# Kernel tuning notes

Hardware: AMD Instinct MI355X
Metric: run time of the kernel (lower is better)

Reference implementation:

```python
import math
import jax, jax.numpy as jnp
import numpy as np

D = 1024
NH = 16
DH = D // NH


def setup_inputs() -> dict:
    key = jax.random.key(0)
    k1, k2, k3 = jax.random.split(key, 3)
    x = jax.random.normal(k1, (2, 2048, D), dtype=jnp.float32)
    s = 1.0 / math.sqrt(D)
    W_qkv = jax.random.normal(k2, (D, 3 * D), dtype=jnp.float32) * s
    W_o = jax.random.normal(k3, (D, D), dtype=jnp.float32) * s
    return {"x": x, "W_qkv": W_qkv, "W_o": W_o}


def _rope(q, k, base=10000.0):
    # q, k: [B, H, T, dh]
    half = q.shape[-1] // 2
    freqs = jnp.arange(half, dtype=q.dtype) / half
    theta = 1.0 / base ** freqs                      # [half]
    t = jnp.arange(q.shape[-2], dtype=q.dtype)       # [T]
    ang = t[:, None] * theta[None, :]                # [T, half]
    cos = jnp.cos(ang)[None, None, :, :]
    sin = jnp.sin(ang)[None, None, :, :]

    def rot(x):
        x1, x2 = x[..., :half], x[..., half:]
        return jnp.concatenate([x1 * cos - x2 * sin, x1 * sin + x2 * cos], axis=-1)

    return rot(q), rot(k)


def reference(x, W_qkv, W_o):
    B, T, d = x.shape
    qkv = x @ W_qkv                                   # [B, T, 3D]
    q, k, v = jnp.split(qkv, 3, axis=-1)
    q = q.reshape(B, T, NH, DH).transpose(0, 2, 1, 3)  # [B, H, T, dh]
    k = k.reshape(B, T, NH, DH).transpose(0, 2, 1, 3)
    v = v.reshape(B, T, NH, DH).transpose(0, 2, 1, 3)
    q, k = _rope(q, k)
    att = jnp.einsum('bhtd,bhsd->bhts', q, k) / math.sqrt(DH)  # [B, H, T, T]
    mask = jnp.triu(jnp.full((T, T), -jnp.inf, dtype=att.dtype), 1)
    att = att + mask
    w = jax.nn.softmax(att, axis=-1)
    y = jnp.einsum('bhts,bhsd->bhtd', w, v)           # [B, H, T, dh]
    y = y.transpose(0, 2, 1, 3).reshape(B, T, d)
    return y @ W_o
```

## Files before the change

### kernel.cpp

```cpp
#include <hip/hip_runtime.h>

typedef __bf16 bf16x8 __attribute__((ext_vector_type(8)));
typedef float f32x4 __attribute__((ext_vector_type(4)));
typedef float f32x16 __attribute__((ext_vector_type(16)));

constexpr int SEQ = 2048;
constexpr int DMODEL = 1024;

#define GLL(gp, lp)                                                              \
  __builtin_amdgcn_global_load_lds((const __attribute__((address_space(1))) void*)(gp), \
                                   (__attribute__((address_space(3))) void*)(lp), 16, 0, 0)

__global__ __launch_bounds__(256) void prep_kernel(const float* __restrict__ x,
                                                   const float* __restrict__ Wqkv,
                                                   const float* __restrict__ Wo,
                                                   __bf16* __restrict__ xbf,
                                                   __bf16* __restrict__ WqkvT,
                                                   __bf16* __restrict__ WoT,
                                                   float2* __restrict__ sct) {
  __shared__ __bf16 tile[64][72];
  int blk = blockIdx.x, t = threadIdx.x;

  if (blk < 256) {
    int i = blk * 256 + t;
    int tt = i >> 5, j = i & 31;
    float theta = exp2f(-(float)j * 0.41524101186092953f);
    float s, c;
    __sincosf((float)tt * theta, &s, &c);
    sct[i] = make_float2(c, s);
    return;
  }
  if (blk >= 1280) {
    size_t i = (size_t)(blk - 1280) * 256 + t;
    const float* sp = x + i * 8;
    float4 f0 = *reinterpret_cast<const float4*>(sp);
    float4 f1 = *reinterpret_cast<const float4*>(sp + 4);
    alignas(16) __bf16 tmp[8];
    tmp[0] = (__bf16)f0.x; tmp[1] = (__bf16)f0.y; tmp[2] = (__bf16)f0.z; tmp[3] = (__bf16)f0.w;
    tmp[4] = (__bf16)f1.x; tmp[5] = (__bf16)f1.y; tmp[6] = (__bf16)f1.z; tmp[7] = (__bf16)f1.w;
    *reinterpret_cast<uint4*>(xbf + i * 8) = *reinterpret_cast<const uint4*>(tmp);
    return;
  }
  const float* src;
  __bf16* dst;
  int C, R, c0, r0;
  if (blk < 512) {
    int idx = blk - 256;
    src = Wo; dst = WoT; R = 1024; C = 1024;
    c0 = (idx & 15) * 64; r0 = (idx >> 4) * 64;
  } else {
    int idx = blk - 512;
    src = Wqkv; dst = WqkvT; R = 1024; C = 3072;
    c0 = (idx % 48) * 64; r0 = (idx / 48) * 64;
  }
#pragma unroll
  for (int p = 0; p < 2; ++p) {
    int flat = p * 256 + t;
    int i = flat >> 3;
    int j8 = (flat & 7) * 8;
    const float* sp = &src[(size_t)(r0 + i) * C + c0 + j8];
    float4 f0 = *reinterpret_cast<const float4*>(sp);
    float4 f1 = *reinterpret_cast<const float4*>(sp + 4);
    tile[i][j8 + 0] = (__bf16)f0.x; tile[i][j8 + 1] = (__bf16)f0.y;
    tile[i][j8 + 2] = (__bf16)f0.z; tile[i][j8 + 3] = (__bf16)f0.w;
    tile[i][j8 + 4] = (__bf16)f1.x; tile[i][j8 + 5] = (__bf16)f1.y;
    tile[i][j8 + 6] = (__bf16)f1.z; tile[i][j8 + 7] = (__bf16)f1.w;
  }
  __syncthreads();
#pragma unroll
  for (int p = 0; p < 2; ++p) {
    int flat = p * 256 + t;
    int i = flat >> 3;
    int j8 = (flat & 7) * 8;
    alignas(16) __bf16 tmp[8];
#pragma unroll
    for (int jj = 0; jj < 8; ++jj) tmp[jj] = tile[j8 + jj][i];
    *reinterpret_cast<uint4*>(&dst[(size_t)(c0 + i) * R + r0 + j8]) =
        *reinterpret_cast<const uint4*>(tmp);
  }
}

template <typename CT, int BN, int MODE>
__global__ __launch_bounds__(512, 6) void gemm_bt_lds(const __bf16* __restrict__ A,
                                                      const __bf16* __restrict__ BT,
                                                      CT* __restrict__ C,
                                                      int M, int N, int K, int lda, int ldc,
                                                      const float2* __restrict__ sct,
                                                      __bf16* __restrict__ vt) {
  constexpr int NF = BN / 32;
  __shared__ __align__(16) __bf16 AB_lds[128 + BN][64];
  __bf16 (*A_lds)[64] = &AB_lds[0];
  __bf16 (*B_lds)[64] = &AB_lds[128];

  int tid = threadIdx.x;
  int lane = tid & 63, w = tid >> 6;
  int g = lane >> 4, l15 = lane & 15;
  int wr = w & 3;
  int wc = w >> 2;
  int m0 = blockIdx.x * 128;
  int n0 = blockIdx.y * BN;
  int r8 = lane >> 3, scol = (lane & 7) * 8;

  const __bf16* ag = A + (size_t)(m0 + w * 16 + r8) * lda + scol;
  const __bf16* bg = BT + (size_t)(n0 + w * (BN / 8) + r8) * K + scol;

  f32x4 acc[2][NF] = {};

  for (int k0 = 0; k0 < K; k0 += 64) {
    __syncthreads();
    GLL(ag + k0, &A_lds[w * 16][0]);
    GLL(ag + (size_t)8 * lda + k0, &A_lds[w * 16 + 8][0]);
    if constexpr (BN == 128) {
      GLL(bg + k0, &B_lds[w * 16][0]);
      GLL(bg + (size_t)8 * K + k0, &B_lds[w * 16 + 8][0]);
    } else {
      GLL(bg + k0, &B_lds[w * 8][0]);
    }
    __syncthreads();
#pragma unroll
    for (int kk = 0; kk < 2; ++kk) {
      bf16x8 a[2], bb[NF];
#pragma unroll
      for (int m = 0; m < 2; ++m)
        a[m] = *reinterpret_cast<const bf16x8*>(&A_lds[wr * 32 + m * 16 + l15][kk * 32 + g * 8]);
#pragma unroll
      for (int n = 0; n < NF; ++n)
        bb[n] = *reinterpret_cast<const bf16x8*>(&B_lds[wc * (BN / 2) + n * 16 + l15][kk * 32 + g * 8]);
#pragma unroll
      for (int m = 0; m < 2; ++m)
#pragma unroll
        for (int n = 0; n < NF; ++n)
          acc[m][n] = __builtin_amdgcn_mfma_f32_16x16x32_bf16(a[m], bb[n], acc[m][n], 0, 0, 0);
    }
  }

  if constexpr (MODE == 3) {
    if (n0 >= 2048) {
      __bf16 (*T_lds)[72] = reinterpret_cast<__bf16(*)[72]>(&AB_lds[0][0]);
      int b = m0 >> 11;
      int s_base = m0 & (SEQ - 1);
#pragma unroll
      for (int half = 0; half < 2; ++half) {
        __syncthreads();
        if (wc == half) {
#pragma unroll
          for (int m = 0; m < 2; ++m)
#pragma unroll
            for (int n = 0; n < NF; ++n)
#pragma unroll
              for (int r = 0; r < 4; ++r)
                T_lds[wr * 32 + m * 16 + 4 * g + r][n * 16 + l15] = (__bf16)acc[m][n][r];
        }
        __syncthreads();
        int head = ((n0 - 2048) >> 6) + half;
        int bh = b * 16 + head;
        int d = tid >> 3;
        int s8 = (tid & 7) * 16;
        __bf16* dst = vt + (size_t)bh * 64 * SEQ + (size_t)d * SEQ + s_base + s8;
#pragma unroll
        for (int j = 0; j < 2; ++j) {
          alignas(16) __bf16 tmp[8];
#pragma unroll
          for (int e = 0; e < 8; ++e) tmp[e] = T_lds[s8 + j * 8 + e][d];
          *reinterpret_cast<uint4*>(dst + j * 8) = *reinterpret_cast<const uint4*>(tmp);
        }
      }
      return;
    }
    bool isq = (n0 < 1024);
    float sc = isq ? 0.18033688011112042f : 1.0f;
#pragma unroll
    for (int m = 0; m < 2; ++m)
#pragma unroll
      for (int r = 0; r < 4; ++r) {
        int row = m0 + wr * 32 + m * 16 + 4 * g + r;
        int t = row & (SEQ - 1);
#pragma unroll
        for (int n = 0; n < 2; ++n) {
          int j = n * 16 + l15;
          float2 cs = sct[(t << 5) + j];
          float x1 = acc[m][n][r], x2 = acc[m][n + 2][r];
          acc[m][n][r]     = (x1 * cs.x - x2 * cs.y) * sc;
          acc[m][n + 2][r] = (x1 * cs.y + x2 * cs.x) * sc;
        }
      }
  }

#pragma unroll
  for (int m = 0; m < 2; ++m)
#pragma unroll
    for (int n = 0; n < NF; ++n)
#pragma unroll
      for (int r = 0; r < 4; ++r) {
        int row = m0 + wr * 32 + m * 16 + 4 * g + r;
        int col = n0 + wc * (BN / 2) + n * 16 + l15;
        C[(size_t)row * ldc + col] = (CT)acc[m][n][r];
      }
}

__device__ inline uint32_t pkbf(float a, float b) {
  union { __bf16 h[2]; uint32_t u; } z;
  z.h[0] = (__bf16)a; z.h[1] = (__bf16)b;
  return z.u;
}

__device__ inline __bf16* slot_base(int gi, __bf16* qkv, __bf16* xbf, int q_local) {
  if (gi < 1024)
    return qkv + (size_t)(gi * 4 + (q_local >> 4)) * 3072 + 2048 + (q_local & 15) * 64;
  return xbf + (size_t)(gi - 1024) * 4096 + (size_t)q_local * 64;
}

__global__ __launch_bounds__(128, 3) void attn_kernel(__bf16* __restrict__ qkv,
                                                      const __bf16* __restrict__ vt,
                                                      __bf16* __restrict__ xbf,
                                                      float* __restrict__ pml) {
  __shared__ __align__(16) __bf16 K_lds[2][64][64];

  int tid = threadIdx.x;
  int w = tid >> 6, lane = tid & 63;
  int l31 = lane & 31, hi = lane >> 5;
  int bid = blockIdx.x;
  int it = bid >> 5, bh = bid & 31;
  int b = bh >> 4, h = bh & 15;

  int qc = 31 - (it >> 1);
  int half = it & 1;
  int NTf = qc + 1;
  int hs = (NTf + 1) >> 1;
  int kv0 = half ? hs : 0;
  int kv1 = half ? NTf : hs;
  int NT = kv1 - kv0;

  __bf16* qbase = qkv + (size_t)b * SEQ * 3072 + h * 64;
  const __bf16* kbase = qbase + 1024;
  const __bf16* vtb = vt + (size_t)bh * 64 * SEQ;

  int q_g = qc * 64 + w * 32 + l31;

  int r8 = lane >> 3;
  int cxe = 8 * ((lane & 7) ^ r8);

  auto STAGE = [&](int bufv, int t) {
#pragma unroll
    for (int i = 0; i < 4; ++i) {
      int R = w * 32 + i * 8;
      GLL(kbase + (size_t)(t * 64 + R + r8) * 3072 + cxe, &K_lds[bufv][R][0]);
    }
  };

  bf16x8 qf[4];
#pragma unroll
  for (int ds = 0; ds < 4; ++ds)
    qf[ds] = *reinterpret_cast<const bf16x8*>(qbase + (size_t)q_g * 3072 + ds * 16 + 8 * hi);

  f32x16 oacc[2] = {};
  float l_run = 0.f;
  const float MFIX = 8.0f;

  if (NT > 0) STAGE(0, kv0);
  __syncthreads();

  int buf = 0;
  for (int jb = 0; jb < NT; ++jb) {
    int kt_g = kv0 + jb;
    bool pre = (jb + 1 < NT);
    if (pre) STAGE(buf ^ 1, kt_g + 1);

    uint4 vr[8];
#pragma unroll
    for (int dt = 0; dt < 2; ++dt)
#pragma unroll
      for (int ks = 0; ks < 4; ++ks)
        vr[dt * 4 + ks] = *reinterpret_cast<const uint4*>(
            vtb + (size_t)(dt * 32 + l31) * SEQ + kt_g * 64 + ks * 16 + 8 * hi);

    f32x16 sacc[2] = {};
    __builtin_amdgcn_s_setprio(1);
#pragma unroll
    for (int kt = 0; kt < 2; ++kt) {
#pragma unroll
      for (int ds = 0; ds < 4; ++ds) {
        bf16x8 kf = *reinterpret_cast<const bf16x8*>(
            &K_lds[buf][kt * 32 + l31][(ds * 16 + 8 * hi) ^ ((l31 & 7) * 8)]);
        sacc[kt] = __builtin_amdgcn_mfma_f32_32x32x16_bf16(kf, qf[ds], sacc[kt], 0, 0, 0);
      }
    }
    __builtin_amdgcn_s_setprio(0);

    if (kt_g == qc) {
#pragma unroll
      for (int kt = 0; kt < 2; ++kt)
#pragma unroll
        for (int r = 0; r < 16; ++r) {
          int k_g = kt_g * 64 + kt * 32 + (r & 3) + 8 * (r >> 2) + 4 * hi;
          if (k_g > q_g) sacc[kt][r] = -1e30f;
        }
    }

    float s0 = 0.f, s1 = 0.f, s2 = 0.f, s3 = 0.f;
#pragma unroll
    for (int kt = 0; kt < 2; ++kt) {
#pragma unroll
      for (int r = 0; r < 16; r += 4) {
        float p0 = exp2f(sacc[kt][r + 0] - MFIX);
        float p1 = exp2f(sacc[kt][r + 1] - MFIX);
        float p2 = exp2f(sacc[kt][r + 2] - MFIX);
        float p3 = exp2f(sacc[kt][r + 3] - MFIX);
        sacc[kt][r + 0] = p0; sacc[kt][r + 1] = p1;
        sacc[kt][r + 2] = p2; sacc[kt][r + 3] = p3;
        s0 += p0; s1 += p1; s2 += p2; s3 += p3;
      }
    }
    float sum = (s0 + s1) + (s2 + s3);
    sum += __shfl_xor(sum, 32);
    l_run += sum;

    uint4 pa[4];
#pragma unroll
    for (int ks = 0; ks < 4; ++ks) {
      int v0 = 2 * ks, v1 = v0 + 1;
      int t0 = v0 >> 2, rb0 = 4 * (v0 & 3);
      int t1 = v1 >> 2, rb1 = 4 * (v1 & 3);
      uint32_t a01, a23, b01, b23;
      if (t0 == 0) { a01 = pkbf(sacc[0][rb0 + 0], sacc[0][rb0 + 1]);
                     a23 = pkbf(sacc[0][rb0 + 2], sacc[0][rb0 + 3]); }
      else         { a01 = pkbf(sacc[1][rb0 + 0], sacc[1][rb0 + 1]);
                     a23 = pkbf(sacc[1][rb0 + 2], sacc[1][rb0 + 3]); }
      if (t1 == 0) { b01 = pkbf(sacc[0][rb1 + 0], sacc[0][rb1 + 1]);
                     b23 = pkbf(sacc[0][rb1 + 2], sacc[0][rb1 + 3]); }
      else         { b01 = pkbf(sacc[1][rb1 + 0], sacc[1][rb1 + 1]);
                     b23 = pkbf(sacc[1][rb1 + 2], sacc[1][rb1 + 3]); }
      uint32_t t01 = hi ? a01 : b01;
      uint32_t t23 = hi ? a23 : b23;
      uint32_t r01 = __shfl_xor(t01, 32);
      uint32_t r23 = __shfl_xor(t23, 32);
      uint32_t k01 = hi ? b01 : a01;
      uint32_t k23 = hi ? b23 : a23;
      pa[ks].x = hi ? r01 : k01;
      pa[ks].y = hi ? r23 : k23;
      pa[ks].z = hi ? k01 : r01;
      pa[ks].w = hi ? k23 : r23;
    }

    __builtin_amdgcn_s_setprio(1);
#pragma unroll
    for (int dt = 0; dt < 2; ++dt) {
#pragma unroll
      for (int ks = 0; ks < 4; ++ks) {
        oacc[dt] = __builtin_amdgcn_mfma_f32_32x32x16_bf16(
            *reinterpret_cast<const bf16x8*>(&vr[dt * 4 + ks]),
            *reinterpret_cast<const bf16x8*>(&pa[ks]), oacc[dt], 0, 0, 0);
      }
    }
    __builtin_amdgcn_s_setprio(0);

    if (pre) {
      asm volatile("s_waitcnt vmcnt(0)" ::: "memory");
      __syncthreads();
    }
    buf ^= 1;
  }

  int gi = ((31 - qc) * 2 + half) * 32 + bh;
  int q_local = w * 32 + l31;
  __bf16* pobase = slot_base(gi, qkv, xbf, q_local);
#pragma unroll
  for (int dt = 0; dt < 2; ++dt)
#pragma unroll
    for (int u = 0; u < 4; ++u) {
      int d0 = dt * 32 + 8 * u + 4 * hi;
      alignas(8) __bf16 tmp[4];
#pragma unroll
      for (int m = 0; m < 4; ++m) tmp[m] = (__bf16)oacc[dt][4 * u + m];
      *reinterpret_cast<uint2*>(pobase + d0) = *reinterpret_cast<const uint2*>(tmp);
    }
  if (hi == 0) pml[gi * 128 + q_local] = l_run;
}

__global__ __launch_bounds__(128) void combine_kernel(__bf16* __restrict__ qkv,
                                                      __bf16* __restrict__ xbf,
                                                      const float* __restrict__ pml) {
  int bid = blockIdx.x;
  int qc = 31 - (bid >> 5), bh = bid & 31;
  int b = bh >> 4, h = bh & 15;
  int t = threadIdx.x;
  int q = t >> 1, dh = (t & 1) * 32;

  int g0 = ((31 - qc) * 2 + 0) * 32 + bh;
  int g1 = g0 + 32;
  float l0 = pml[g0 * 128 + q];
  float l1 = pml[g1 * 128 + q];
  float inv = 1.0f / (l0 + l1);

  const __bf16* p0 = slot_base(g0, qkv, xbf, q) + dh;
  const __bf16* p1 = slot_base(g1, qkv, xbf, q) + dh;
  __bf16* yq = qkv + (size_t)(b * SEQ + qc * 64 + q) * 3072 + h * 64 + dh;

#pragma unroll
  for (int c = 0; c < 4; ++c) {
    uint4 ua = *reinterpret_cast<const uint4*>(p0 + c * 8);
    uint4 ub = *reinterpret_cast<const uint4*>(p1 + c * 8);
    const __bf16* va = reinterpret_cast<const __bf16*>(&ua);
    const __bf16* vb = reinterpret_cast<const __bf16*>(&ub);
    alignas(16) __bf16 outv[8];
#pragma unroll
    for (int j = 0; j < 8; ++j)
      outv[j] = (__bf16)((((float)va[j]) + ((float)vb[j])) * inv);
    *reinterpret_cast<uint4*>(yq + c * 8) = *reinterpret_cast<const uint4*>(outv);
  }
}

extern "C" void kernel_launch(void* const* d_in, const int* in_sizes, int n_in,
                              void* d_out, int out_size, void* d_ws, size_t ws_size,
                              hipStream_t stream) {
  const float* x = (const float*)d_in[0];
  const float* Wqkv = (const float*)d_in[1];
  const float* Wo = (const float*)d_in[2];
  float* out = (float*)d_out;

  __bf16* ws = (__bf16*)d_ws;
  __bf16* WqkvT = ws;
  __bf16* WoT = WqkvT + (size_t)3072 * 1024;
  __bf16* qkv = WoT + (size_t)1024 * 1024;
  __bf16* xbf = qkv + (size_t)4096 * 3072;
  __bf16* vtb = xbf + (size_t)4096 * 1024;
  float* pml = (float*)(vtb + (size_t)32 * 64 * SEQ);
  float2* sct = (float2*)(pml + 2048 * 128);

  prep_kernel<<<3328, 256, 0, stream>>>(x, Wqkv, Wo, xbf, WqkvT, WoT, sct);

  gemm_bt_lds<__bf16, 128, 3><<<dim3(32, 24), 512, 0, stream>>>(
      xbf, WqkvT, qkv, 4096, 3072, 1024, 1024, 3072, sct, vtb);

  attn_kernel<<<2048, 128, 0, stream>>>(qkv, vtb, xbf, pml);

  combine_kernel<<<1024, 128, 0, stream>>>(qkv, xbf, pml);

  gemm_bt_lds<float, 64, 0><<<dim3(32, 16), 512, 0, stream>>>(
      qkv, WoT, out, 4096, 1024, 1024, 3072, 1024, sct, nullptr);
}
```

Measured before the change: 132.5 us.

## Split causal attention KV range into up to five balanced parts per query chunk

Instead of splitting every query chunk's KV range into two halves, each chunk is split into ceil((qc+1)/7) parts so each work item handles at most about 7 KV tiles. This yields 90 items per head instead of 64, which balances work and shortens the longest blocks in the causal schedule. The combine kernel now sums a variable number of partial outputs and denominators. Extra partial buffers reuse the WqkvT region and a new tail region in workspace, which adds memory traffic and combine work.

```diff
diff --git a/kernel.cpp b/kernel.cpp
--- a/kernel.cpp
+++ b/kernel.cpp
@@ -10,6 +10,31 @@
 #define GLL(gp, lp)                                                              \
   __builtin_amdgcn_global_load_lds((const __attribute__((address_space(1))) void*)(gp), \
                                    (__attribute__((address_space(3))) void*)(lp), 16, 0, 0)
+
+constexpr int N_ITEMS = 90;
+constexpr int P_MAX = 5;
+struct AttnMaps {
+  signed char qc[N_ITEMS];
+  signed char part[N_ITEMS];
+  signed char parts[32];
+  short ibase[32];
+};
+constexpr AttnMaps buildMaps() {
+  AttnMaps m = {};
+  int idx = 0;
+  for (int qc = 31; qc >= 0; --qc) {
+    int p = (qc + 1 + 6) / 7;
+    m.parts[qc] = (signed char)p;
+    m.ibase[qc] = (short)idx;
+    for (int i = 0; i < p; ++i) {
+      m.qc[idx] = (signed char)qc;
+      m.part[idx] = (signed char)i;
+      ++idx;
+    }
+  }
+  return m;
+}
+constexpr AttnMaps AM = buildMaps();
 
 __global__ __launch_bounds__(256) void prep_kernel(const float* __restrict__ x,
                                                    const float* __restrict__ Wqkv,
@@ -204,15 +229,20 @@
   return z.u;
 }
 
-__device__ inline __bf16* slot_base(int gi, __bf16* qkv, __bf16* xbf, int q_local) {
+__device__ inline __bf16* slot_base(int gi, __bf16* qkv, __bf16* xbf,
+                                    __bf16* wqkvt, __bf16* ptail, int q_local) {
   if (gi < 1024)
     return qkv + (size_t)(gi * 4 + (q_local >> 4)) * 3072 + 2048 + (q_local & 15) * 64;
-  return xbf + (size_t)(gi - 1024) * 4096 + (size_t)q_local * 64;
+  if (gi < 2048) return xbf + (size_t)(gi - 1024) * 4096 + (size_t)q_local * 64;
+  if (gi < 2816) return wqkvt + (size_t)(gi - 2048) * 4096 + (size_t)q_local * 64;
+  return ptail + (size_t)(gi - 2816) * 4096 + (size_t)q_local * 64;
 }
 
 __global__ __launch_bounds__(128, 3) void attn_kernel(__bf16* __restrict__ qkv,
                                                       const __bf16* __restrict__ vt,
                                                       __bf16* __restrict__ xbf,
+                                                      __bf16* __restrict__ wqkvt,
+                                                      __bf16* __restrict__ ptail,
                                                       float* __restrict__ pml) {
   __shared__ __align__(16) __bf16 K_lds[2][64][64];
 
@@ -223,13 +253,13 @@
   int it = bid >> 5, bh = bid & 31;
   int b = bh >> 4, h = bh & 15;
 
-  int qc = 31 - (it >> 1);
-  int half = it & 1;
+  int qc = AM.qc[it];
+  int part = AM.part[it];
+  int p = AM.parts[qc];
   int NTf = qc + 1;
-  int hs = (NTf + 1) >> 1;
-  int kv0 = half ? hs : 0;
-  int kv1 = half ? NTf : hs;
-  int NT = kv1 - kv0;
+  int base = NTf / p, rem = NTf - base * p;
+  int kv0 = part * base + (part < rem ? part : rem);
+  int NT = base + (part < rem ? 1 : 0);
 
   __bf16* qbase = qkv + (size_t)b * SEQ * 3072 + h * 64;
   const __bf16* kbase = qbase + 1024;
@@ -257,7 +287,7 @@
   float l_run = 0.f;
   const float MFIX = 8.0f;
 
-  if (NT > 0) STAGE(0, kv0);
+  STAGE(0, kv0);
   __syncthreads();
 
   int buf = 0;
@@ -361,9 +391,9 @@
     buf ^= 1;
   }
 
-  int gi = ((31 - qc) * 2 + half) * 32 + bh;
+  int gi = it * 32 + bh;
   int q_local = w * 32 + l31;
-  __bf16* pobase = slot_base(gi, qkv, xbf, q_local);
+  __bf16* pobase = slot_base(gi, qkv, xbf, wqkvt, ptail, q_local);
 #pragma unroll
   for (int dt = 0; dt < 2; ++dt)
 #pragma unroll
@@ -379,33 +409,40 @@
 
 __global__ __launch_bounds__(128) void combine_kernel(__bf16* __restrict__ qkv,
                                                       __bf16* __restrict__ xbf,
+                                                      __bf16* __restrict__ wqkvt,
+                                                      __bf16* __restrict__ ptail,
                                                       const float* __restrict__ pml) {
   int bid = blockIdx.x;
   int qc = 31 - (bid >> 5), bh = bid & 31;
   int b = bh >> 4, h = bh & 15;
+  int p = AM.parts[qc];
+  int ib = AM.ibase[qc];
   int t = threadIdx.x;
   int q = t >> 1, dh = (t & 1) * 32;
 
-  int g0 = ((31 - qc) * 2 + 0) * 32 + bh;
-  int g1 = g0 + 32;
-  float l0 = pml[g0 * 128 + q];
-  float l1 = pml[g1 * 128 + q];
-  float inv = 1.0f / (l0 + l1);
-
-  const __bf16* p0 = slot_base(g0, qkv, xbf, q) + dh;
-  const __bf16* p1 = slot_base(g1, qkv, xbf, q) + dh;
+  float lsum = 0.f;
+#pragma unroll
+  for (int i = 0; i < P_MAX; ++i)
+    if (i < p) lsum += pml[((ib + i) * 32 + bh) * 128 + q];
+  float inv = 1.0f / lsum;
+
   __bf16* yq = qkv + (size_t)(b * SEQ + qc * 64 + q) * 3072 + h * 64 + dh;
-
 #pragma unroll
   for (int c = 0; c < 4; ++c) {
-    uint4 ua = *reinterpret_cast<const uint4*>(p0 + c * 8);
-    uint4 ub = *reinterpret_cast<const uint4*>(p1 + c * 8);
-    const __bf16* va = reinterpret_cast<const __bf16*>(&ua);
-    const __bf16* vb = reinterpret_cast<const __bf16*>(&ub);
+    float accv[8] = {};
+#pragma unroll
+    for (int i = 0; i < P_MAX; ++i) {
+      if (i < p) {
+        const __bf16* po = slot_base((ib + i) * 32 + bh, qkv, xbf, wqkvt, ptail, q) + dh + c * 8;
+        uint4 u = *reinterpret_cast<const uint4*>(po);
+        const __bf16* v = reinterpret_cast<const __bf16*>(&u);
+#pragma unroll
+        for (int j = 0; j < 8; ++j) accv[j] += (float)v[j];
+      }
+    }
     alignas(16) __bf16 outv[8];
 #pragma unroll
-    for (int j = 0; j < 8; ++j)
-      outv[j] = (__bf16)((((float)va[j]) + ((float)vb[j])) * inv);
+    for (int j = 0; j < 8; ++j) outv[j] = (__bf16)(accv[j] * inv);
     *reinterpret_cast<uint4*>(yq + c * 8) = *reinterpret_cast<const uint4*>(outv);
   }
 }
@@ -425,16 +462,17 @@
   __bf16* xbf = qkv + (size_t)4096 * 3072;
   __bf16* vtb = xbf + (size_t)4096 * 1024;
   float* pml = (float*)(vtb + (size_t)32 * 64 * SEQ);
-  float2* sct = (float2*)(pml + 2048 * 128);
+  float2* sct = (float2*)(pml + (size_t)2880 * 128);
+  __bf16* ptail = (__bf16*)(sct + 2048 * 32);
 
   prep_kernel<<<3328, 256, 0, stream>>>(x, Wqkv, Wo, xbf, WqkvT, WoT, sct);
 
   gemm_bt_lds<__bf16, 128, 3><<<dim3(32, 24), 512, 0, stream>>>(
       xbf, WqkvT, qkv, 4096, 3072, 1024, 1024, 3072, sct, vtb);
 
-  attn_kernel<<<2048, 128, 0, stream>>>(qkv, vtb, xbf, pml);
-
-  combine_kernel<<<1024, 128, 0, stream>>>(qkv, xbf, pml);
+  attn_kernel<<<N_ITEMS * 32, 128, 0, stream>>>(qkv, vtb, xbf, WqkvT, ptail, pml);
+
+  combine_kernel<<<1024, 128, 0, stream>>>(qkv, xbf, WqkvT, ptail, pml);
 
   gemm_bt_lds<float, 64, 0><<<dim3(32, 16), 512, 0, stream>>>(
       qkv, WoT, out, 4096, 1024, 1024, 3072, 1024, sct, nullptr);
```

Measured after the change: 141.1 us. 6.6% more time.
